# Optimization experiments

Hardware: AMD Instinct MI355X
Metric: run time of the kernel (lower is better)

Reference implementation:

```python
import jax, jax.numpy as jnp
import numpy as np

N, B, D, Q = 32, 36, 2048, 1024  # batch, objects, v_dim, q_dim


def setup_inputs() -> dict:
    key = jax.random.key(0)
    ks = jax.random.split(key, 6)
    sc = 0.02  # small init so ReLU chains stay well-scaled
    return {
        "v": jax.random.normal(ks[0], (N, B, D), jnp.float32),
        "q": jax.random.normal(ks[1], (N, Q), jnp.float32),
        "W1": jax.random.normal(ks[2], (D, D), jnp.float32) * sc,
        "b1": jnp.zeros((D,), jnp.float32),
        "W2": jax.random.normal(ks[3], (D, D), jnp.float32) * sc,
        "b2": jnp.zeros((D,), jnp.float32),
        "W3": jax.random.normal(ks[4], (Q, D), jnp.float32) * sc,
        "b3": jnp.zeros((D,), jnp.float32),
    }


def reference(v, q, W1, b1, W2, b2, W3, b3):
    # FCNet = ReLU(Linear(.)) with weight-norm folded, dropout=0 (eval).
    # Original calls linear3 twice (linear4 unused bug), so q_emb == q_emb2.
    qe = jax.nn.relu(q @ W3 + b3)  # (N, D)
    # pairs[n,i,j] = v[n,i]*qe[n] + v[n,j]*qe[n]  -> (N, B, B, D)
    pairs = (v[:, :, None, :] + v[:, None, :, :]) * qe[:, None, None, :]
    h = jax.nn.relu(jnp.einsum('nijd,de->nije', pairs, W1) + b1)  # linear1
    x = jnp.sum(h, axis=2)  # sum over j relations -> (N, B, D)
    return jax.nn.relu(x @ W2 + b2)  # linear2
```

## Files before the change

kernel.cpp:

```cpp
#include <hip/hip_runtime.h>
#include <stdint.h>

#define N_BATCH 32
#define B_OBJ   36
#define D_DIM   2048
#define Q_DIM   1024

typedef __bf16 bf16x8 __attribute__((ext_vector_type(8)));
typedef float  f32x4  __attribute__((ext_vector_type(4)));

__device__ __forceinline__ uint16_t f2bf(float f) {
    uint32_t u = __builtin_bit_cast(uint32_t, f);
    uint32_t r = (u + 0x7FFFu + ((u >> 16) & 1u)) >> 16;
    return (uint16_t)r;
}

__device__ __forceinline__ void gld_lds16(const void* g, void* l) {
    __builtin_amdgcn_global_load_lds(
        (const __attribute__((address_space(1))) uint32_t*)g,
        (__attribute__((address_space(3))) uint32_t*)l, 16, 0, 0);
}

__global__ __launch_bounds__(256) void transpose_all(
    const float* __restrict__ W1, const float* __restrict__ W2,
    const float* __restrict__ W3,
    uint16_t* __restrict__ W1t, uint16_t* __restrict__ W2t,
    uint16_t* __restrict__ W3t) {
    __shared__ float tile[64][65];
    int gy = blockIdx.y;
    const float* W; uint16_t* Wt; int K, k0;
    if (gy < 32)      { W = W1; Wt = W1t; K = 2048; k0 = gy * 64; }
    else if (gy < 64) { W = W2; Wt = W2t; K = 2048; k0 = (gy - 32) * 64; }
    else              { W = W3; Wt = W3t; K = 1024; k0 = (gy - 64) * 64; }
    int n0 = blockIdx.x * 64;
    int t = threadIdx.x;
    {
        int r = t >> 4, c = (t & 15) * 4;
#pragma unroll
        for (int p = 0; p < 4; ++p)
            *(float4*)&tile[r + p * 16][c] =
                *(const float4*)&W[(size_t)(k0 + r + p * 16) * 2048 + n0 + c];
    }
    __syncthreads();
    {
        int n = t >> 2, kb = (t & 3) * 16;
#pragma unroll
        for (int g4 = 0; g4 < 4; ++g4) {
            int k = kb + g4 * 4;
            ushort4 o;
            o.x = f2bf(tile[k][n]);     o.y = f2bf(tile[k + 1][n]);
            o.z = f2bf(tile[k + 2][n]); o.w = f2bf(tile[k + 3][n]);
            *(ushort4*)&Wt[(size_t)(n0 + n) * K + k0 + k] = o;
        }
    }
}

__global__ __launch_bounds__(256) void qk_gemm(
    const float* __restrict__ q,
    const uint16_t* __restrict__ W3t,
    float* __restrict__ qpart) {
    __shared__ __align__(16) uint16_t As[32][32];
    __shared__ __align__(16) uint16_t Bs[128][32];
    int t = threadIdx.x, lane = t & 63, wave = t >> 6;
    int l15 = lane & 15, quad = lane >> 4;
    int n0 = blockIdx.x * 128;
    int kbase = blockIdx.y * 256;
    f32x4 acc[2][2] = {};
    int ar = t >> 3, ac = (t & 7) * 4;
    int br = t >> 2, bk = (t & 3) * 8;

    for (int k0 = 0; k0 < 256; k0 += 32) {
        __syncthreads();
        float4 av = *(const float4*)&q[(size_t)ar * Q_DIM + kbase + k0 + ac];
        ushort4 a4;
        a4.x = f2bf(av.x); a4.y = f2bf(av.y); a4.z = f2bf(av.z); a4.w = f2bf(av.w);
        *(ushort4*)&As[ar][ac] = a4;
        *(uint4*)&Bs[br][bk]      = *(const uint4*)&W3t[(size_t)(n0 + br) * Q_DIM + kbase + k0 + bk];
        *(uint4*)&Bs[br + 64][bk] = *(const uint4*)&W3t[(size_t)(n0 + br + 64) * Q_DIM + kbase + k0 + bk];
        __syncthreads();
        bf16x8 af[2], bfr[2];
        af[0]  = *(const bf16x8*)&As[l15][quad * 8];
        af[1]  = *(const bf16x8*)&As[16 + l15][quad * 8];
        bfr[0] = *(const bf16x8*)&Bs[wave * 32 + l15][quad * 8];
        bfr[1] = *(const bf16x8*)&Bs[wave * 32 + 16 + l15][quad * 8];
#pragma unroll
        for (int i = 0; i < 2; ++i)
#pragma unroll
            for (int j = 0; j < 2; ++j)
                acc[i][j] = __builtin_amdgcn_mfma_f32_16x16x32_bf16(af[i], bfr[j], acc[i][j], 0, 0, 0);
    }
    float* dst = qpart + (size_t)blockIdx.y * 32 * D_DIM;
#pragma unroll
    for (int i = 0; i < 2; ++i)
#pragma unroll
        for (int j = 0; j < 2; ++j) {
            int n = n0 + wave * 32 + j * 16 + l15;
#pragma unroll
            for (int r = 0; r < 4; ++r)
                dst[(size_t)(i * 16 + quad * 4 + r) * D_DIM + n] = acc[i][j][r];
        }
}

__global__ __launch_bounds__(256) void qe_makeu(
    const float* __restrict__ qpart, const float* __restrict__ b3,
    const float* __restrict__ v, uint16_t* __restrict__ u) {
    int n = blockIdx.y;
    int c4 = blockIdx.x * 256 + threadIdx.x;
    const float4* p = (const float4*)qpart;
    size_t base = (size_t)n * 512 + c4;
    float4 s0 = p[base], s1 = p[16384 + base], s2 = p[32768 + base], s3 = p[49152 + base];
    float4 b = ((const float4*)b3)[c4];
    float4 qe;
    qe.x = fmaxf(s0.x + s1.x + s2.x + s3.x + b.x, 0.f);
    qe.y = fmaxf(s0.y + s1.y + s2.y + s3.y + b.y, 0.f);
    qe.z = fmaxf(s0.z + s1.z + s2.z + s3.z + b.z, 0.f);
    qe.w = fmaxf(s0.w + s1.w + s2.w + s3.w + b.w, 0.f);
    const float4* v4 = (const float4*)v + (size_t)n * B_OBJ * 512 + c4;
    ushort4* u4 = (ushort4*)u + (size_t)n * B_OBJ * 512 + c4;
#pragma unroll 4
    for (int i = 0; i < B_OBJ; ++i) {
        float4 vv = v4[(size_t)i * 512];
        ushort4 o;
        o.x = f2bf(vv.x * qe.x); o.y = f2bf(vv.y * qe.y);
        o.z = f2bf(vv.z * qe.z); o.w = f2bf(vv.w * qe.w);
        u4[(size_t)i * 512] = o;
    }
}

__global__ __launch_bounds__(256) void gemm_batch(
    const uint16_t* __restrict__ A,
    const uint16_t* __restrict__ Bt,
    const float* __restrict__ bias,
    void* __restrict__ Cv,
    int mode) {
    __shared__ __align__(16) float smemf[13312];
    uint16_t* As = (uint16_t*)smemf;
    uint16_t* Bs = As + 10240;
    float* yt = smemf;

    int t = threadIdx.x, lane = t & 63, wave = t >> 6;
    int l15 = lane & 15, quad = lane >> 4;
    int bg = blockIdx.y;
    int n0 = blockIdx.x * 128;
    const uint16_t* Ab = A + (size_t)bg * 72 * D_DIM;

    const uint16_t* gp[13]; uint16_t* lp[13];
#pragma unroll
    for (int c = 0; c < 13; ++c) {
        int r = wave * 13 + c;
        int row16 = lane >> 2, kin = (lane & 3) * 8;
        if (r < 20) {
            int h = r / 5, g = r % 5;
            gp[c] = Ab + (size_t)(g * 16 + row16) * D_DIM + h * 32 + kin;
            lp[c] = As + h * 2560 + g * 512;
        } else {
            int rb = r - 20, h = rb >> 3, g = rb & 7;
            gp[c] = Bt + (size_t)(n0 + g * 16 + row16) * D_DIM + h * 32 + kin;
            lp[c] = Bs + h * 4096 + g * 512;
        }
    }

    f32x4 acc[5][2] = {};

    for (int k0 = 0; k0 < D_DIM; k0 += 128) {
        __syncthreads();
#pragma unroll
        for (int c = 0; c < 13; ++c) gld_lds16(gp[c] + k0, lp[c]);
        __syncthreads();
#pragma unroll
        for (int s = 0; s < 4; ++s) {
            bf16x8 af[5], bfr[2];
#pragma unroll
            for (int i = 0; i < 5; ++i)
                af[i] = *(const bf16x8*)(As + s * 2560 + (i * 16 + l15) * 32 + quad * 8);
#pragma unroll
            for (int j = 0; j < 2; ++j)
                bfr[j] = *(const bf16x8*)(Bs + s * 4096 + (wave * 32 + j * 16 + l15) * 32 + quad * 8);
#pragma unroll
            for (int i = 0; i < 5; ++i)
#pragma unroll
                for (int j = 0; j < 2; ++j)
                    acc[i][j] = __builtin_amdgcn_mfma_f32_16x16x32_bf16(af[i], bfr[j], acc[i][j], 0, 0, 0);
        }
    }

    if (mode == 0) {
        uint16_t* X = (uint16_t*)Cv;
        __syncthreads();
#pragma unroll
        for (int i = 0; i < 5; ++i)
#pragma unroll
            for (int r = 0; r < 4; ++r) {
                int row = i * 16 + quad * 4 + r;
                if (row < 72)
#pragma unroll
                    for (int j = 0; j < 2; ++j)
                        yt[row * 132 + wave * 32 + j * 16 + l15] = acc[i][j][r];
            }
        __syncthreads();
        int col = t & 127, half = t >> 7;
        float b = bias[n0 + col];
        float z[36];
#pragma unroll
        for (int j2 = 0; j2 < 36; ++j2) z[j2] = yt[(half * 36 + j2) * 132 + col];
        int batch = bg * 2 + half;
#pragma unroll
        for (int i2 = 0; i2 < 36; ++i2) {
            float zi = z[i2] + b;
            float s = 0.f;
#pragma unroll
            for (int j2 = 0; j2 < 36; ++j2) s += fmaxf(zi + z[j2], 0.f);
            X[(size_t)(batch * 36 + i2) * D_DIM + n0 + col] = f2bf(s);
        }
    } else {
        float* O = (float*)Cv;
#pragma unroll
        for (int i = 0; i < 5; ++i)
#pragma unroll
            for (int r = 0; r < 4; ++r) {
                int row = i * 16 + quad * 4 + r;
                if (row < 72)
#pragma unroll
                    for (int j = 0; j < 2; ++j) {
                        int cc = n0 + wave * 32 + j * 16 + l15;
                        O[(size_t)(bg * 72 + row) * D_DIM + cc] =
                            fmaxf(acc[i][j][r] + bias[cc], 0.f);
                    }
            }
    }
}

extern "C" void kernel_launch(void* const* d_in, const int* in_sizes, int n_in,
                              void* d_out, int out_size, void* d_ws, size_t ws_size,
                              hipStream_t stream) {
    const float* v  = (const float*)d_in[0];
    const float* q  = (const float*)d_in[1];
    const float* W1 = (const float*)d_in[2];
    const float* b1 = (const float*)d_in[3];
    const float* W2 = (const float*)d_in[4];
    const float* b2 = (const float*)d_in[5];
    const float* W3 = (const float*)d_in[6];
    const float* b3 = (const float*)d_in[7];
    float* out = (float*)d_out;

    char* ws = (char*)d_ws;
    uint16_t* W1t   = (uint16_t*)(ws + 0);
    uint16_t* W2t   = (uint16_t*)(ws + 8388608);
    uint16_t* W3t   = (uint16_t*)(ws + 16777216);
    uint16_t* u     = (uint16_t*)(ws + 16777216);
    float*    qpart = (float*)   (ws + 21495808);
    uint16_t* x     = (uint16_t*)(ws + 22806528);

    transpose_all<<<dim3(32, 80), 256, 0, stream>>>(W1, W2, W3, W1t, W2t, W3t);

    qk_gemm<<<dim3(16, 4), 256, 0, stream>>>(q, W3t, qpart);

    qe_makeu<<<dim3(2, N_BATCH), 256, 0, stream>>>(qpart, b3, v, u);

    gemm_batch<<<dim3(16, 16), 256, 0, stream>>>(u, W1t, b1, x, 0);

    gemm_batch<<<dim3(16, 16), 256, 0, stream>>>(x, W2t, b2, out, 1);
}
```

Baseline: 187.9 us.

## Restructure GEMMs with split-K double-buffered tiles and separate pair-sum/reduce kernels

Replaces the 72-row batched GEMM with a 128x64 tiled split-K (2-way) GEMM that double-buffers its LDS loads, writing fp32 partials that are reduced by new pair-sum and output-reduction kernels. The q@W3 product now runs as a plain fp32 split-K kernel reading W3 directly, so W3 no longer needs a transpose pass. The intent is more blocks in flight and overlap of global loads with MFMA work. The cost is extra fp32 partial traffic and two additional launches.

```diff
diff --git a/kernel.cpp b/kernel.cpp
--- a/kernel.cpp
+++ b/kernel.cpp
@@ -23,15 +23,12 @@
 
 __global__ __launch_bounds__(256) void transpose_all(
     const float* __restrict__ W1, const float* __restrict__ W2,
-    const float* __restrict__ W3,
-    uint16_t* __restrict__ W1t, uint16_t* __restrict__ W2t,
-    uint16_t* __restrict__ W3t) {
+    uint16_t* __restrict__ W1t, uint16_t* __restrict__ W2t) {
     __shared__ float tile[64][65];
     int gy = blockIdx.y;
-    const float* W; uint16_t* Wt; int K, k0;
-    if (gy < 32)      { W = W1; Wt = W1t; K = 2048; k0 = gy * 64; }
-    else if (gy < 64) { W = W2; Wt = W2t; K = 2048; k0 = (gy - 32) * 64; }
-    else              { W = W3; Wt = W3t; K = 1024; k0 = (gy - 64) * 64; }
+    const float* W; uint16_t* Wt; int k0;
+    if (gy < 32) { W = W1; Wt = W1t; k0 = gy * 64; }
+    else         { W = W2; Wt = W2t; k0 = (gy - 32) * 64; }
     int n0 = blockIdx.x * 64;
     int t = threadIdx.x;
     {
@@ -50,55 +47,41 @@
             ushort4 o;
             o.x = f2bf(tile[k][n]);     o.y = f2bf(tile[k + 1][n]);
             o.z = f2bf(tile[k + 2][n]); o.w = f2bf(tile[k + 3][n]);
-            *(ushort4*)&Wt[(size_t)(n0 + n) * K + k0 + k] = o;
-        }
-    }
-}
-
-__global__ __launch_bounds__(256) void qk_gemm(
-    const float* __restrict__ q,
-    const uint16_t* __restrict__ W3t,
+            *(ushort4*)&Wt[(size_t)(n0 + n) * 2048 + k0 + k] = o;
+        }
+    }
+}
+
+__global__ __launch_bounds__(256) void qe_f32(
+    const float* __restrict__ q, const float* __restrict__ W3,
     float* __restrict__ qpart) {
-    __shared__ __align__(16) uint16_t As[32][32];
-    __shared__ __align__(16) uint16_t Bs[128][32];
-    int t = threadIdx.x, lane = t & 63, wave = t >> 6;
-    int l15 = lane & 15, quad = lane >> 4;
-    int n0 = blockIdx.x * 128;
-    int kbase = blockIdx.y * 256;
-    f32x4 acc[2][2] = {};
-    int ar = t >> 3, ac = (t & 7) * 4;
-    int br = t >> 2, bk = (t & 3) * 8;
-
-    for (int k0 = 0; k0 < 256; k0 += 32) {
-        __syncthreads();
-        float4 av = *(const float4*)&q[(size_t)ar * Q_DIM + kbase + k0 + ac];
-        ushort4 a4;
-        a4.x = f2bf(av.x); a4.y = f2bf(av.y); a4.z = f2bf(av.z); a4.w = f2bf(av.w);
-        *(ushort4*)&As[ar][ac] = a4;
-        *(uint4*)&Bs[br][bk]      = *(const uint4*)&W3t[(size_t)(n0 + br) * Q_DIM + kbase + k0 + bk];
-        *(uint4*)&Bs[br + 64][bk] = *(const uint4*)&W3t[(size_t)(n0 + br + 64) * Q_DIM + kbase + k0 + bk];
-        __syncthreads();
-        bf16x8 af[2], bfr[2];
-        af[0]  = *(const bf16x8*)&As[l15][quad * 8];
-        af[1]  = *(const bf16x8*)&As[16 + l15][quad * 8];
-        bfr[0] = *(const bf16x8*)&Bs[wave * 32 + l15][quad * 8];
-        bfr[1] = *(const bf16x8*)&Bs[wave * 32 + 16 + l15][quad * 8];
-#pragma unroll
-        for (int i = 0; i < 2; ++i)
-#pragma unroll
-            for (int j = 0; j < 2; ++j)
-                acc[i][j] = __builtin_amdgcn_mfma_f32_16x16x32_bf16(af[i], bfr[j], acc[i][j], 0, 0, 0);
-    }
-    float* dst = qpart + (size_t)blockIdx.y * 32 * D_DIM;
-#pragma unroll
-    for (int i = 0; i < 2; ++i)
-#pragma unroll
-        for (int j = 0; j < 2; ++j) {
-            int n = n0 + wave * 32 + j * 16 + l15;
-#pragma unroll
-            for (int r = 0; r < 4; ++r)
-                dst[(size_t)(i * 16 + quad * 4 + r) * D_DIM + n] = acc[i][j][r];
-        }
+    __shared__ float qs[128][32];
+    int t = threadIdx.x;
+    int e0 = blockIdx.x * 64;
+    int kbase = blockIdx.y * 128;
+    {
+        int nn = t >> 3, kg = (t & 7) * 16;
+#pragma unroll
+        for (int p = 0; p < 4; ++p) {
+            float4 f = *(const float4*)&q[(size_t)nn * Q_DIM + kbase + kg + p * 4];
+            qs[kg + p * 4 + 0][nn] = f.x; qs[kg + p * 4 + 1][nn] = f.y;
+            qs[kg + p * 4 + 2][nn] = f.z; qs[kg + p * 4 + 3][nn] = f.w;
+        }
+    }
+    __syncthreads();
+    int n = t >> 3, e8 = (t & 7) * 8;
+    float acc[8] = {};
+#pragma unroll 4
+    for (int k = 0; k < 128; ++k) {
+        float qv = qs[k][n];
+        float4 wa = *(const float4*)&W3[(size_t)(kbase + k) * D_DIM + e0 + e8];
+        float4 wb = *(const float4*)&W3[(size_t)(kbase + k) * D_DIM + e0 + e8 + 4];
+        acc[0] += qv * wa.x; acc[1] += qv * wa.y; acc[2] += qv * wa.z; acc[3] += qv * wa.w;
+        acc[4] += qv * wb.x; acc[5] += qv * wb.y; acc[6] += qv * wb.z; acc[7] += qv * wb.w;
+    }
+    float* dst = qpart + (size_t)blockIdx.y * 32 * D_DIM + (size_t)n * D_DIM + e0 + e8;
+    *(float4*)dst = *(float4*)&acc[0];
+    *(float4*)(dst + 4) = *(float4*)&acc[4];
 }
 
 __global__ __launch_bounds__(256) void qe_makeu(
@@ -108,13 +91,16 @@
     int c4 = blockIdx.x * 256 + threadIdx.x;
     const float4* p = (const float4*)qpart;
     size_t base = (size_t)n * 512 + c4;
-    float4 s0 = p[base], s1 = p[16384 + base], s2 = p[32768 + base], s3 = p[49152 + base];
+    float4 s = p[base];
+#pragma unroll
+    for (int z = 1; z < 8; ++z) {
+        float4 sz = p[(size_t)z * 16384 + base];
+        s.x += sz.x; s.y += sz.y; s.z += sz.z; s.w += sz.w;
+    }
     float4 b = ((const float4*)b3)[c4];
     float4 qe;
-    qe.x = fmaxf(s0.x + s1.x + s2.x + s3.x + b.x, 0.f);
-    qe.y = fmaxf(s0.y + s1.y + s2.y + s3.y + b.y, 0.f);
-    qe.z = fmaxf(s0.z + s1.z + s2.z + s3.z + b.z, 0.f);
-    qe.w = fmaxf(s0.w + s1.w + s2.w + s3.w + b.w, 0.f);
+    qe.x = fmaxf(s.x + b.x, 0.f); qe.y = fmaxf(s.y + b.y, 0.f);
+    qe.z = fmaxf(s.z + b.z, 0.f); qe.w = fmaxf(s.w + b.w, 0.f);
     const float4* v4 = (const float4*)v + (size_t)n * B_OBJ * 512 + c4;
     ushort4* u4 = (ushort4*)u + (size_t)n * B_OBJ * 512 + c4;
 #pragma unroll 4
@@ -127,107 +113,117 @@
     }
 }
 
-__global__ __launch_bounds__(256) void gemm_batch(
+__global__ __launch_bounds__(256) void gemm_ks(
     const uint16_t* __restrict__ A,
     const uint16_t* __restrict__ Bt,
-    const float* __restrict__ bias,
-    void* __restrict__ Cv,
-    int mode) {
-    __shared__ __align__(16) float smemf[13312];
-    uint16_t* As = (uint16_t*)smemf;
-    uint16_t* Bs = As + 10240;
-    float* yt = smemf;
-
+    float* __restrict__ Yp) {
+    __shared__ __align__(16) uint16_t sm[24576];
     int t = threadIdx.x, lane = t & 63, wave = t >> 6;
     int l15 = lane & 15, quad = lane >> 4;
-    int bg = blockIdx.y;
-    int n0 = blockIdx.x * 128;
-    const uint16_t* Ab = A + (size_t)bg * 72 * D_DIM;
-
-    const uint16_t* gp[13]; uint16_t* lp[13];
-#pragma unroll
-    for (int c = 0; c < 13; ++c) {
-        int r = wave * 13 + c;
+    int wr = wave >> 1, wc = wave & 1;
+    int n0 = blockIdx.x * 64, m0 = blockIdx.y * 128, kz = blockIdx.z;
+    const uint16_t* Ab = A  + (size_t)m0 * D_DIM + kz * 1024;
+    const uint16_t* Bb = Bt + (size_t)n0 * D_DIM + kz * 1024;
+
+    const uint16_t* gp[6]; uint16_t* lp[6]; int ofs[6];
+#pragma unroll
+    for (int c = 0; c < 6; ++c) {
+        int r = wave + 4 * c;
         int row16 = lane >> 2, kin = (lane & 3) * 8;
-        if (r < 20) {
-            int h = r / 5, g = r % 5;
+        if (r < 16) {
+            int h = r >> 3, g = r & 7;
             gp[c] = Ab + (size_t)(g * 16 + row16) * D_DIM + h * 32 + kin;
-            lp[c] = As + h * 2560 + g * 512;
+            lp[c] = sm + h * 4096 + g * 512;
+            ofs[c] = 8192;
         } else {
-            int rb = r - 20, h = rb >> 3, g = rb & 7;
-            gp[c] = Bt + (size_t)(n0 + g * 16 + row16) * D_DIM + h * 32 + kin;
-            lp[c] = Bs + h * 4096 + g * 512;
-        }
-    }
-
-    f32x4 acc[5][2] = {};
-
-    for (int k0 = 0; k0 < D_DIM; k0 += 128) {
+            int rb = r - 16, h = rb >> 2, g = rb & 3;
+            gp[c] = Bb + (size_t)(g * 16 + row16) * D_DIM + h * 32 + kin;
+            lp[c] = sm + 16384 + h * 2048 + g * 512;
+            ofs[c] = 4096;
+        }
+    }
+
+    f32x4 acc[4][2] = {};
+
+#pragma unroll
+    for (int c = 0; c < 6; ++c) gld_lds16(gp[c], lp[c]);
+
+    for (int it = 0; it < 16; ++it) {
+        int buf = it & 1;
         __syncthreads();
-#pragma unroll
-        for (int c = 0; c < 13; ++c) gld_lds16(gp[c] + k0, lp[c]);
-        __syncthreads();
-#pragma unroll
-        for (int s = 0; s < 4; ++s) {
-            bf16x8 af[5], bfr[2];
-#pragma unroll
-            for (int i = 0; i < 5; ++i)
-                af[i] = *(const bf16x8*)(As + s * 2560 + (i * 16 + l15) * 32 + quad * 8);
+        if (it < 15) {
+            int nxt = buf ^ 1;
+#pragma unroll
+            for (int c = 0; c < 6; ++c)
+                gld_lds16(gp[c] + (it + 1) * 64, lp[c] + nxt * ofs[c]);
+        }
+#pragma unroll
+        for (int s = 0; s < 2; ++s) {
+            bf16x8 af[4], bfr[2];
+#pragma unroll
+            for (int i = 0; i < 4; ++i)
+                af[i] = *(const bf16x8*)(sm + buf * 8192 + s * 4096 +
+                                         (wr * 64 + i * 16 + l15) * 32 + quad * 8);
 #pragma unroll
             for (int j = 0; j < 2; ++j)
-                bfr[j] = *(const bf16x8*)(Bs + s * 4096 + (wave * 32 + j * 16 + l15) * 32 + quad * 8);
-#pragma unroll
-            for (int i = 0; i < 5; ++i)
+                bfr[j] = *(const bf16x8*)(sm + 16384 + buf * 4096 + s * 2048 +
+                                          (wc * 32 + j * 16 + l15) * 32 + quad * 8);
+#pragma unroll
+            for (int i = 0; i < 4; ++i)
 #pragma unroll
                 for (int j = 0; j < 2; ++j)
                     acc[i][j] = __builtin_amdgcn_mfma_f32_16x16x32_bf16(af[i], bfr[j], acc[i][j], 0, 0, 0);
         }
     }
 
-    if (mode == 0) {
-        uint16_t* X = (uint16_t*)Cv;
-        __syncthreads();
-#pragma unroll
-        for (int i = 0; i < 5; ++i)
-#pragma unroll
-            for (int r = 0; r < 4; ++r) {
-                int row = i * 16 + quad * 4 + r;
-                if (row < 72)
-#pragma unroll
-                    for (int j = 0; j < 2; ++j)
-                        yt[row * 132 + wave * 32 + j * 16 + l15] = acc[i][j][r];
-            }
-        __syncthreads();
-        int col = t & 127, half = t >> 7;
-        float b = bias[n0 + col];
-        float z[36];
-#pragma unroll
-        for (int j2 = 0; j2 < 36; ++j2) z[j2] = yt[(half * 36 + j2) * 132 + col];
-        int batch = bg * 2 + half;
-#pragma unroll
-        for (int i2 = 0; i2 < 36; ++i2) {
-            float zi = z[i2] + b;
-            float s = 0.f;
-#pragma unroll
-            for (int j2 = 0; j2 < 36; ++j2) s += fmaxf(zi + z[j2], 0.f);
-            X[(size_t)(batch * 36 + i2) * D_DIM + n0 + col] = f2bf(s);
-        }
-    } else {
-        float* O = (float*)Cv;
-#pragma unroll
-        for (int i = 0; i < 5; ++i)
-#pragma unroll
-            for (int r = 0; r < 4; ++r) {
-                int row = i * 16 + quad * 4 + r;
-                if (row < 72)
-#pragma unroll
-                    for (int j = 0; j < 2; ++j) {
-                        int cc = n0 + wave * 32 + j * 16 + l15;
-                        O[(size_t)(bg * 72 + row) * D_DIM + cc] =
-                            fmaxf(acc[i][j][r] + bias[cc], 0.f);
-                    }
-            }
-    }
+    float* Y = Yp + (size_t)kz * 1152 * D_DIM;
+#pragma unroll
+    for (int i = 0; i < 4; ++i)
+#pragma unroll
+        for (int j = 0; j < 2; ++j) {
+            int col = n0 + wc * 32 + j * 16 + l15;
+#pragma unroll
+            for (int r = 0; r < 4; ++r)
+                Y[(size_t)(m0 + wr * 64 + i * 16 + quad * 4 + r) * D_DIM + col] = acc[i][j][r];
+        }
+}
+
+__global__ __launch_bounds__(256) void pairsum_red(
+    const float* __restrict__ Yp, const float* __restrict__ b1,
+    uint16_t* __restrict__ X) {
+    int n = blockIdx.y;
+    int d = blockIdx.x * 256 + threadIdx.x;
+    const float* y0 = Yp + (size_t)(n * B_OBJ) * D_DIM + d;
+    const float* y1 = y0 + (size_t)1152 * D_DIM;
+    float z[B_OBJ];
+#pragma unroll
+    for (int j = 0; j < B_OBJ; ++j)
+        z[j] = y0[(size_t)j * D_DIM] + y1[(size_t)j * D_DIM];
+    float b = b1[d];
+    uint16_t* xb = X + (size_t)(n * B_OBJ) * D_DIM + d;
+#pragma unroll
+    for (int i = 0; i < B_OBJ; ++i) {
+        float zi = z[i] + b;
+        float s = 0.f;
+#pragma unroll
+        for (int j = 0; j < B_OBJ; ++j) s += fmaxf(zi + z[j], 0.f);
+        xb[(size_t)i * D_DIM] = f2bf(s);
+    }
+}
+
+__global__ __launch_bounds__(256) void reduce_out(
+    const float* __restrict__ Op, const float* __restrict__ b2,
+    float* __restrict__ out) {
+    int i = blockIdx.x * 256 + threadIdx.x;
+    const float4* p = (const float4*)Op;
+    float4 a = p[i], b = p[589824 + i];
+    float4 bb = ((const float4*)b2)[i & 511];
+    float4 o;
+    o.x = fmaxf(a.x + b.x + bb.x, 0.f);
+    o.y = fmaxf(a.y + b.y + bb.y, 0.f);
+    o.z = fmaxf(a.z + b.z + bb.z, 0.f);
+    o.w = fmaxf(a.w + b.w + bb.w, 0.f);
+    ((float4*)out)[i] = o;
 }
 
 extern "C" void kernel_launch(void* const* d_in, const int* in_sizes, int n_in,
@@ -246,18 +242,20 @@
     char* ws = (char*)d_ws;
     uint16_t* W1t   = (uint16_t*)(ws + 0);
     uint16_t* W2t   = (uint16_t*)(ws + 8388608);
-    uint16_t* W3t   = (uint16_t*)(ws + 16777216);
     uint16_t* u     = (uint16_t*)(ws + 16777216);
     float*    qpart = (float*)   (ws + 21495808);
-    uint16_t* x     = (uint16_t*)(ws + 22806528);
-
-    transpose_all<<<dim3(32, 80), 256, 0, stream>>>(W1, W2, W3, W1t, W2t, W3t);
-
-    qk_gemm<<<dim3(16, 4), 256, 0, stream>>>(q, W3t, qpart);
-
+    uint16_t* x     = (uint16_t*)(ws + 23592960);
+    float*    Yp    = (float*)   (ws + 28311552);
+    float*    Op    = Yp;
+
+    transpose_all<<<dim3(32, 64), 256, 0, stream>>>(W1, W2, W1t, W2t);
+
+    qe_f32<<<dim3(32, 8), 256, 0, stream>>>(q, W3, qpart);
     qe_makeu<<<dim3(2, N_BATCH), 256, 0, stream>>>(qpart, b3, v, u);
 
-    gemm_batch<<<dim3(16, 16), 256, 0, stream>>>(u, W1t, b1, x, 0);
-
-    gemm_batch<<<dim3(16, 16), 256, 0, stream>>>(x, W2t, b2, out, 1);
-}
+    gemm_ks<<<dim3(32, 9, 2), 256, 0, stream>>>(u, W1t, Yp);
+    pairsum_red<<<dim3(8, N_BATCH), 256, 0, stream>>>(Yp, b1, x);
+
+    gemm_ks<<<dim3(32, 9, 2), 256, 0, stream>>>(x, W2t, Op);
+    reduce_out<<<2304, 256, 0, stream>>>(Op, b2, out);
+}
```

Result: no change. 185.8 us (-1.1%).
